# Optimization experiments

Measured on AMD Instinct MI355X. Metric: run time of the kernel, lower is better.

Reference implementation:

```python
import jax, jax.numpy as jnp
import numpy as np

D_MODEL = 1024
NUM_HEADS = 16
D_K = D_MODEL // NUM_HEADS


def setup_inputs() -> dict:
    key = jax.random.key(0)
    ks = jax.random.split(key, 11)
    B, S = 4, 2048
    scale = 1.0 / np.sqrt(D_MODEL)
    inp = {
        'query': jax.random.normal(ks[0], (B, S, D_MODEL), jnp.float32),
        'key': jax.random.normal(ks[1], (B, S, D_MODEL), jnp.float32),
        'value': jax.random.normal(ks[2], (B, S, D_MODEL), jnp.float32),
        'Wq': jax.random.normal(ks[3], (D_MODEL, D_MODEL), jnp.float32) * scale,
        'bq': jnp.zeros((D_MODEL,), jnp.float32),
        'Wk': jax.random.normal(ks[4], (D_MODEL, D_MODEL), jnp.float32) * scale,
        'bk': jnp.zeros((D_MODEL,), jnp.float32),
        'Wv': jax.random.normal(ks[5], (D_MODEL, D_MODEL), jnp.float32) * scale,
        'bv': jnp.zeros((D_MODEL,), jnp.float32),
        'Wo': jax.random.normal(ks[6], (D_MODEL, D_MODEL), jnp.float32) * scale,
        'bo': jnp.zeros((D_MODEL,), jnp.float32),
    }
    return inp


def _split_heads(x):
    # [B, S, D] -> [B, H, S, d_k]
    B, S, _ = x.shape
    return x.reshape(B, S, NUM_HEADS, D_K).transpose(0, 2, 1, 3)


def reference(query, key, value, Wq, bq, Wk, bk, Wv, bv, Wo, bo):
    # torch nn.Linear: y = x @ W.T + b
    q = _split_heads(query @ Wq.T + bq)   # [B,H,Sq,dk]
    k = _split_heads(key @ Wk.T + bk)     # [B,H,Sk,dk]
    v = _split_heads(value @ Wv.T + bv)   # [B,H,Sk,dk]
    scores = jnp.einsum('bhqd,bhkd->bhqk', q, k) / jnp.sqrt(jnp.float32(D_K))
    attn = jax.nn.softmax(scores, axis=-1)
    out = jnp.einsum('bhqk,bhkd->bhqd', attn, v)  # [B,H,Sq,dk]
    B, H, Sq, dk = out.shape
    out = out.transpose(0, 2, 1, 3).reshape(B, Sq, D_MODEL)
    return out @ Wo.T + bo
```

## Files before the change

kernel.cpp:

```cpp
#include <hip/hip_runtime.h>

typedef short bf16x8 __attribute__((ext_vector_type(8)));
typedef float f32x4 __attribute__((ext_vector_type(4)));
typedef unsigned short u16;

#define S_LEN 2048
#define DM 1024
#define NH 16
#define DK 64
#define BHD ((size_t)S_LEN * DK)

#define QSCALE 0.18033688011112042f

static __device__ __forceinline__ u16 f2bf(float f) {
  union { float f; unsigned u; } x; x.f = f;
  unsigned r = x.u + 0x7FFFu + ((x.u >> 16) & 1u);
  return (u16)(r >> 16);
}

static __device__ __forceinline__ void gload_lds16(const u16* g, u16* l) {
  __builtin_amdgcn_global_load_lds(
      (const __attribute__((address_space(1))) unsigned int*)g,
      (__attribute__((address_space(3))) unsigned int*)l, 16, 0, 0);
}

__global__ __launch_bounds__(256) void conv_all(
    const float* __restrict__ q, const float* __restrict__ k, const float* __restrict__ v,
    const float* __restrict__ Wq, const float* __restrict__ Wk,
    const float* __restrict__ Wv, const float* __restrict__ Wo,
    u16* __restrict__ xq, u16* __restrict__ xk, u16* __restrict__ xv,
    u16* __restrict__ wb) {
  const int b = blockIdx.x;
  const float* s; u16* d; float sc = 1.0f; int i;
  if (b < 8192) {
    s = q; d = xq; sc = QSCALE; i = b * 256 + threadIdx.x;
  } else if (b < 16384) {
    s = k; d = xk; i = (b - 8192) * 256 + threadIdx.x;
  } else if (b < 24576) {
    s = v; d = xv; i = (b - 16384) * 256 + threadIdx.x;
  } else {
    int b2 = b - 24576, wsel = b2 >> 10;
    s = (wsel == 0) ? Wq : (wsel == 1) ? Wk : (wsel == 2) ? Wv : Wo;
    d = wb + (size_t)wsel * 1048576;
    i = (b2 & 1023) * 256 + threadIdx.x;
  }
  float4 vv = ((const float4*)s)[i];
  ushort4 h;
  h.x = f2bf(vv.x * sc); h.y = f2bf(vv.y * sc);
  h.z = f2bf(vv.z * sc); h.w = f2bf(vv.w * sc);
  ((ushort4*)d)[i] = h;
}

#define GSTAGE(DST, SRC)                                                          \
  {                                                                               \
    _Pragma("unroll") for (int j = 0; j < 4; ++j) {                               \
      gload_lds16((SRC) + (size_t)(j * 32 + (w << 3) + (l >> 3)) * 1024 +         \
                      (size_t)(((l & 7) ^ (l >> 3)) * 8),                         \
                  (DST) + (j * 256 + w * 64) * 8);                                \
    }                                                                             \
  }

__global__ __launch_bounds__(256) void proj_gemm(
    const u16* __restrict__ xq, const u16* __restrict__ xk, const u16* __restrict__ xv,
    const u16* __restrict__ wb,
    const float* __restrict__ bq, const float* __restrict__ bk, const float* __restrict__ bv,
    u16* __restrict__ qws, u16* __restrict__ kws, u16* __restrict__ vws)
{
  __shared__ u16 Al[2][128 * 64];
  __shared__ u16 Bl[2][128 * 64];
  const int z = blockIdx.z;
  const u16* Xb = (z == 0) ? xq : (z == 1) ? xk : xv;
  const u16* Wb = wb + (size_t)z * 1048576;
  const float* bias = (z == 0) ? bq : (z == 1) ? bk : bv;
  const float bscale = (z == 0) ? QSCALE : 1.0f;

  const int t = threadIdx.x;
  const int l = t & 63, w = t >> 6;
  const int lr = l & 15, lg = l >> 4;
  const int wm = w >> 1, wn = w & 1;
  const int m0 = blockIdx.x * 128, n0 = blockIdx.y * 128;
  const int sxr = lr & 7;

  f32x4 acc[4][4] = {};

  GSTAGE(&Al[0][0], Xb + (size_t)m0 * 1024)
  GSTAGE(&Bl[0][0], Wb + (size_t)n0 * 1024)

  for (int i = 0; i < 16; ++i) {
    __syncthreads();
    if (i < 15) {
      GSTAGE(&Al[(i + 1) & 1][0], Xb + (size_t)m0 * 1024 + (i + 1) * 64)
      GSTAGE(&Bl[(i + 1) & 1][0], Wb + (size_t)n0 * 1024 + (i + 1) * 64)
    }
    const u16* Ab_ = &Al[i & 1][0];
    const u16* Bb_ = &Bl[i & 1][0];

    bf16x8 a[4][2], b[4][2];
#pragma unroll
    for (int mi = 0; mi < 4; ++mi) {
      const u16* rp = Ab_ + (wm * 64 + mi * 16 + lr) * 64;
      a[mi][0] = *(const bf16x8*)(rp + ((lg ^ sxr) * 8));
      a[mi][1] = *(const bf16x8*)(rp + (((4 + lg) ^ sxr) * 8));
    }
#pragma unroll
    for (int ni = 0; ni < 4; ++ni) {
      const u16* rp = Bb_ + (wn * 64 + ni * 16 + lr) * 64;
      b[ni][0] = *(const bf16x8*)(rp + ((lg ^ sxr) * 8));
      b[ni][1] = *(const bf16x8*)(rp + (((4 + lg) ^ sxr) * 8));
    }
    __builtin_amdgcn_s_setprio(1);
#pragma unroll
    for (int mi = 0; mi < 4; ++mi)
#pragma unroll
      for (int ni = 0; ni < 4; ++ni) {
        acc[mi][ni] = __builtin_amdgcn_mfma_f32_16x16x32_bf16(a[mi][0], b[ni][0], acc[mi][ni], 0, 0, 0);
        acc[mi][ni] = __builtin_amdgcn_mfma_f32_16x16x32_bf16(a[mi][1], b[ni][1], acc[mi][ni], 0, 0, 0);
      }
    __builtin_amdgcn_s_setprio(0);
  }

#pragma unroll
  for (int mi = 0; mi < 4; ++mi) {
#pragma unroll
    for (int ni = 0; ni < 4; ++ni) {
#pragma unroll
      for (int r = 0; r < 4; ++r) {
        int m = m0 + wm * 64 + mi * 16 + lg * 4 + r;
        int n = n0 + wn * 64 + ni * 16 + lr;
        float y = acc[mi][ni][r] + bias[n] * bscale;
        u16 h = f2bf(y);
        int b_ = m >> 11, s = m & 2047, hh = n >> 6, d = n & 63;
        size_t head = (size_t)(b_ * NH + hh);
        if (z == 0)      qws[head * BHD + (size_t)s * DK + d] = h;
        else if (z == 1) kws[head * BHD + (size_t)s * DK + d] = h;
        else             vws[head * BHD + (size_t)d * S_LEN + s] = h;
      }
    }
  }
}

__global__ __launch_bounds__(256) void oproj_gemm(
    const u16* __restrict__ Ab, const u16* __restrict__ Wob,
    const float* __restrict__ bo, float* __restrict__ out)
{
  __shared__ u16 Al[2][128 * 64];
  __shared__ u16 Bl[2][128 * 64];
  const int t = threadIdx.x;
  const int l = t & 63, w = t >> 6;
  const int lr = l & 15, lg = l >> 4;
  const int wm = w >> 1, wn = w & 1;
  const int m0 = blockIdx.x * 128, n0 = blockIdx.y * 128;
  const int sxr = lr & 7;

  f32x4 acc[4][4] = {};

  GSTAGE(&Al[0][0], Ab + (size_t)m0 * 1024)
  GSTAGE(&Bl[0][0], Wob + (size_t)n0 * 1024)

  for (int i = 0; i < 16; ++i) {
    __syncthreads();
    if (i < 15) {
      GSTAGE(&Al[(i + 1) & 1][0], Ab + (size_t)m0 * 1024 + (i + 1) * 64)
      GSTAGE(&Bl[(i + 1) & 1][0], Wob + (size_t)n0 * 1024 + (i + 1) * 64)
    }
    const u16* Ab_ = &Al[i & 1][0];
    const u16* Bb_ = &Bl[i & 1][0];

    bf16x8 a[4][2], b[4][2];
#pragma unroll
    for (int mi = 0; mi < 4; ++mi) {
      const u16* rp = Ab_ + (wm * 64 + mi * 16 + lr) * 64;
      a[mi][0] = *(const bf16x8*)(rp + ((lg ^ sxr) * 8));
      a[mi][1] = *(const bf16x8*)(rp + (((4 + lg) ^ sxr) * 8));
    }
#pragma unroll
    for (int ni = 0; ni < 4; ++ni) {
      const u16* rp = Bb_ + (wn * 64 + ni * 16 + lr) * 64;
      b[ni][0] = *(const bf16x8*)(rp + ((lg ^ sxr) * 8));
      b[ni][1] = *(const bf16x8*)(rp + (((4 + lg) ^ sxr) * 8));
    }
    __builtin_amdgcn_s_setprio(1);
#pragma unroll
    for (int mi = 0; mi < 4; ++mi)
#pragma unroll
      for (int ni = 0; ni < 4; ++ni) {
        acc[mi][ni] = __builtin_amdgcn_mfma_f32_16x16x32_bf16(a[mi][0], b[ni][0], acc[mi][ni], 0, 0, 0);
        acc[mi][ni] = __builtin_amdgcn_mfma_f32_16x16x32_bf16(a[mi][1], b[ni][1], acc[mi][ni], 0, 0, 0);
      }
    __builtin_amdgcn_s_setprio(0);
  }

#pragma unroll
  for (int mi = 0; mi < 4; ++mi) {
#pragma unroll
    for (int ni = 0; ni < 4; ++ni) {
#pragma unroll
      for (int r = 0; r < 4; ++r) {
        int m = m0 + wm * 64 + mi * 16 + lg * 4 + r;
        int n = n0 + wn * 64 + ni * 16 + lr;
        out[(size_t)m * DM + n] = acc[mi][ni][r] + bo[n];
      }
    }
  }
}

__global__ __launch_bounds__(256, 4) void attn_kernel(
    const u16* __restrict__ qh, const u16* __restrict__ kh,
    const u16* __restrict__ vt, u16* __restrict__ aout)
{
  __shared__ u16 KT[2][64 * 64];
  __shared__ u16 VT[2][64 * 64];

  const int t = threadIdx.x;
  const int l = t & 63, w = t >> 6;
  const int lr = l & 15, lg = l >> 4;

  const int bid = blockIdx.x;
  const int logical = (bid & 7) * 128 + (bid >> 3);
  const int bh = logical >> 4;
  const int qb = (logical & 15) * 128 + w * 32;

  const u16* qp = qh + (size_t)bh * BHD;
  const u16* kp = kh + (size_t)bh * BHD;
  const u16* vp = vt + (size_t)bh * BHD;
  const int sx = lr & 7;

  const int srow = t >> 3;
  const int scolS = (t & 7) ^ (srow & 7);

  bf16x8 qf[2][2];
#pragma unroll
  for (int qi = 0; qi < 2; ++qi)
#pragma unroll
    for (int c = 0; c < 2; ++c)
      qf[qi][c] = *(const bf16x8*)(qp + (size_t)(qb + qi * 16 + lr) * DK + c * 32 + lg * 8);

  bf16x8 onesf;
#pragma unroll
  for (int e = 0; e < 8; ++e) onesf[e] = (short)0x3F80;

  f32x4 acc[4][2] = {};
  f32x4 acc_l[2] = {};

#define STAGE(B, KV)                                                                  \
  {                                                                                   \
    _Pragma("unroll") for (int j = 0; j < 2; ++j) {                                   \
      gload_lds16(kp + (size_t)((KV) + j * 32 + srow) * DK + scolS * 8,               \
                  &KT[B][j * 2048 + w * 512]);                                        \
      gload_lds16(vp + (size_t)(j * 32 + srow) * S_LEN + (KV) + scolS * 8,            \
                  &VT[B][j * 2048 + w * 512]);                                        \
    }                                                                                 \
  }

  STAGE(0, 0)

  for (int i = 0; i < 32; ++i) {
    __syncthreads();
    if (i < 31) STAGE((i + 1) & 1, (i + 1) * 64)

    const u16* Kb = &KT[i & 1][0];
    const u16* Vb = &VT[i & 1][0];

    f32x4 sc[4][2] = {};
    __builtin_amdgcn_s_setprio(1);
#pragma unroll
    for (int ct = 0; ct < 4; ++ct) {
      bf16x8 k0 = *(const bf16x8*)(Kb + (ct * 16 + lr) * 64 + ((lg ^ sx) * 8));
      bf16x8 k1 = *(const bf16x8*)(Kb + (ct * 16 + lr) * 64 + (((4 + lg) ^ sx) * 8));
      sc[ct][0] = __builtin_amdgcn_mfma_f32_16x16x32_bf16(k0, qf[0][0], sc[ct][0], 0, 0, 0);
      sc[ct][0] = __builtin_amdgcn_mfma_f32_16x16x32_bf16(k1, qf[0][1], sc[ct][0], 0, 0, 0);
      sc[ct][1] = __builtin_amdgcn_mfma_f32_16x16x32_bf16(k0, qf[1][0], sc[ct][1], 0, 0, 0);
      sc[ct][1] = __builtin_amdgcn_mfma_f32_16x16x32_bf16(k1, qf[1][1], sc[ct][1], 0, 0, 0);
    }
    __builtin_amdgcn_s_setprio(0);

    unsigned cpk[2][4][2];
#pragma unroll
    for (int qi = 0; qi < 2; ++qi) {
#pragma unroll
      for (int ct = 0; ct < 4; ++ct) {
        float p0 = __builtin_amdgcn_exp2f(sc[ct][qi][0]);
        float p1 = __builtin_amdgcn_exp2f(sc[ct][qi][1]);
        float p2 = __builtin_amdgcn_exp2f(sc[ct][qi][2]);
        float p3 = __builtin_amdgcn_exp2f(sc[ct][qi][3]);
        asm("v_cvt_pk_bf16_f32 %0, %1, %2" : "=v"(cpk[qi][ct][0]) : "v"(p0), "v"(p1));
        asm("v_cvt_pk_bf16_f32 %0, %1, %2" : "=v"(cpk[qi][ct][1]) : "v"(p2), "v"(p3));
      }
    }

    bf16x8 pf[2][2];
#pragma unroll
    for (int qi = 0; qi < 2; ++qi)
#pragma unroll
      for (int kk = 0; kk < 2; ++kk) {
        unsigned a0 = cpk[qi][2 * kk][0], b0 = cpk[qi][2 * kk + 1][0];
        unsigned a1 = cpk[qi][2 * kk][1], b1 = cpk[qi][2 * kk + 1][1];
        asm("v_permlane32_swap_b32 %0, %1" : "+v"(a0), "+v"(b0));
        asm("v_permlane16_swap_b32 %0, %1" : "+v"(a0), "+v"(b0));
        asm("v_permlane32_swap_b32 %0, %1" : "+v"(a1), "+v"(b1));
        asm("v_permlane16_swap_b32 %0, %1" : "+v"(a1), "+v"(b1));
        union { unsigned u[4]; bf16x8 v; } tmp;
        tmp.u[0] = a0; tmp.u[1] = a1; tmp.u[2] = b0; tmp.u[3] = b1;
        pf[qi][kk] = tmp.v;
      }

    __builtin_amdgcn_s_setprio(1);
    acc_l[0] = __builtin_amdgcn_mfma_f32_16x16x32_bf16(pf[0][0], onesf, acc_l[0], 0, 0, 0);
    acc_l[0] = __builtin_amdgcn_mfma_f32_16x16x32_bf16(pf[0][1], onesf, acc_l[0], 0, 0, 0);
    acc_l[1] = __builtin_amdgcn_mfma_f32_16x16x32_bf16(pf[1][0], onesf, acc_l[1], 0, 0, 0);
    acc_l[1] = __builtin_amdgcn_mfma_f32_16x16x32_bf16(pf[1][1], onesf, acc_l[1], 0, 0, 0);
#pragma unroll
    for (int ni = 0; ni < 4; ++ni) {
      bf16x8 vf0 = *(const bf16x8*)(Vb + (ni * 16 + lr) * 64 + ((lg ^ sx) * 8));
      bf16x8 vf1 = *(const bf16x8*)(Vb + (ni * 16 + lr) * 64 + (((4 + lg) ^ sx) * 8));
      acc[ni][0] = __builtin_amdgcn_mfma_f32_16x16x32_bf16(pf[0][0], vf0, acc[ni][0], 0, 0, 0);
      acc[ni][0] = __builtin_amdgcn_mfma_f32_16x16x32_bf16(pf[0][1], vf1, acc[ni][0], 0, 0, 0);
      acc[ni][1] = __builtin_amdgcn_mfma_f32_16x16x32_bf16(pf[1][0], vf0, acc[ni][1], 0, 0, 0);
      acc[ni][1] = __builtin_amdgcn_mfma_f32_16x16x32_bf16(pf[1][1], vf1, acc[ni][1], 0, 0, 0);
    }
    __builtin_amdgcn_s_setprio(0);
  }
#undef STAGE

  const int b_ = bh >> 4, hh = bh & 15;
#pragma unroll
  for (int qi = 0; qi < 2; ++qi) {
#pragma unroll
    for (int r = 0; r < 4; ++r) {
      float inv = 1.0f / acc_l[qi][r];
      int s = qb + qi * 16 + lg * 4 + r;
#pragma unroll
      for (int ni = 0; ni < 4; ++ni)
        aout[((size_t)(b_ * S_LEN + s)) * DM + hh * DK + ni * 16 + lr] =
            f2bf(acc[ni][qi][r] * inv);
    }
  }
}

extern "C" void kernel_launch(void* const* d_in, const int* in_sizes, int n_in,
                              void* d_out, int out_size, void* d_ws, size_t ws_size,
                              hipStream_t stream) {
  (void)in_sizes; (void)n_in; (void)out_size; (void)ws_size;
  const float* q  = (const float*)d_in[0];
  const float* k  = (const float*)d_in[1];
  const float* v  = (const float*)d_in[2];
  const float* Wq = (const float*)d_in[3];
  const float* bq = (const float*)d_in[4];
  const float* Wk = (const float*)d_in[5];
  const float* bk = (const float*)d_in[6];
  const float* Wv = (const float*)d_in[7];
  const float* bv = (const float*)d_in[8];
  const float* Wo = (const float*)d_in[9];
  const float* bo = (const float*)d_in[10];
  float* out = (float*)d_out;

  u16* qws = (u16*)d_ws;
  u16* kws = qws + (size_t)8388608;
  u16* vws = kws + (size_t)8388608;
  u16* xb  = vws + (size_t)8388608;
  u16* wb  = xb  + (size_t)8388608;
  u16* aws = xb;
  u16* kxb = (u16*)d_out;
  u16* vxb = kxb + (size_t)8388608;

  conv_all<<<dim3(28672), dim3(256), 0, stream>>>(q, k, v, Wq, Wk, Wv, Wo, xb, kxb, vxb, wb);

  proj_gemm<<<dim3(64, 8, 3), dim3(256), 0, stream>>>(xb, kxb, vxb, wb, bq, bk, bv,
                                                      qws, kws, vws);

  attn_kernel<<<dim3(1024), dim3(256), 0, stream>>>(qws, kws, vws, aws);

  oproj_gemm<<<dim3(64, 8), dim3(256), 0, stream>>>(aws, wb + 3145728, bo, out);
}
```

Before: 198.4 us.

## Fuse fp32-to-bf16 activation conversion into the projection GEMM's A-tile staging

```diff
diff --git a/kernel.cpp b/kernel.cpp
--- a/kernel.cpp
+++ b/kernel.cpp
@@ -24,26 +24,16 @@
       (__attribute__((address_space(3))) unsigned int*)l, 16, 0, 0);
 }
 
-__global__ __launch_bounds__(256) void conv_all(
-    const float* __restrict__ q, const float* __restrict__ k, const float* __restrict__ v,
+__global__ __launch_bounds__(256) void conv_w(
     const float* __restrict__ Wq, const float* __restrict__ Wk,
     const float* __restrict__ Wv, const float* __restrict__ Wo,
-    u16* __restrict__ xq, u16* __restrict__ xk, u16* __restrict__ xv,
     u16* __restrict__ wb) {
   const int b = blockIdx.x;
-  const float* s; u16* d; float sc = 1.0f; int i;
-  if (b < 8192) {
-    s = q; d = xq; sc = QSCALE; i = b * 256 + threadIdx.x;
-  } else if (b < 16384) {
-    s = k; d = xk; i = (b - 8192) * 256 + threadIdx.x;
-  } else if (b < 24576) {
-    s = v; d = xv; i = (b - 16384) * 256 + threadIdx.x;
-  } else {
-    int b2 = b - 24576, wsel = b2 >> 10;
-    s = (wsel == 0) ? Wq : (wsel == 1) ? Wk : (wsel == 2) ? Wv : Wo;
-    d = wb + (size_t)wsel * 1048576;
-    i = (b2 & 1023) * 256 + threadIdx.x;
-  }
+  const int wsel = b >> 10;
+  const float* s = (wsel == 0) ? Wq : (wsel == 1) ? Wk : (wsel == 2) ? Wv : Wo;
+  const float sc = (wsel == 0) ? QSCALE : 1.0f;
+  u16* d = wb + (size_t)wsel * 1048576;
+  int i = (b & 1023) * 256 + threadIdx.x;
   float4 vv = ((const float4*)s)[i];
   ushort4 h;
   h.x = f2bf(vv.x * sc); h.y = f2bf(vv.y * sc);
@@ -60,16 +50,39 @@
     }                                                                             \
   }
 
+#define ASTAGE_LOAD(R, SRCF, K0)                                                  \
+  {                                                                               \
+    _Pragma("unroll") for (int j = 0; j < 4; ++j) {                               \
+      const int r_ = j * 32 + (t >> 3);                                           \
+      const int g_ = (t & 7) ^ (r_ & 7);                                          \
+      const float* p_ = (SRCF) + (size_t)(m0 + r_) * 1024 + (K0) + g_ * 8;        \
+      R[j][0] = *(const float4*)(p_);                                             \
+      R[j][1] = *(const float4*)(p_ + 4);                                         \
+    }                                                                             \
+  }
+#define ASTAGE_WRITE(DST, R)                                                      \
+  {                                                                               \
+    _Pragma("unroll") for (int j = 0; j < 4; ++j) {                               \
+      unsigned u0, u1, u2, u3;                                                    \
+      asm("v_cvt_pk_bf16_f32 %0, %1, %2" : "=v"(u0) : "v"(R[j][0].x), "v"(R[j][0].y)); \
+      asm("v_cvt_pk_bf16_f32 %0, %1, %2" : "=v"(u1) : "v"(R[j][0].z), "v"(R[j][0].w)); \
+      asm("v_cvt_pk_bf16_f32 %0, %1, %2" : "=v"(u2) : "v"(R[j][1].x), "v"(R[j][1].y)); \
+      asm("v_cvt_pk_bf16_f32 %0, %1, %2" : "=v"(u3) : "v"(R[j][1].z), "v"(R[j][1].w)); \
+      uint4 pk_; pk_.x = u0; pk_.y = u1; pk_.z = u2; pk_.w = u3;                  \
+      *(uint4*)((DST) + (size_t)(t + j * 256) * 8) = pk_;                         \
+    }                                                                             \
+  }
+
 __global__ __launch_bounds__(256) void proj_gemm(
-    const u16* __restrict__ xq, const u16* __restrict__ xk, const u16* __restrict__ xv,
-    const u16* __restrict__ wb,
+    const float* __restrict__ qf32, const float* __restrict__ kf32,
+    const float* __restrict__ vf32, const u16* __restrict__ wb,
     const float* __restrict__ bq, const float* __restrict__ bk, const float* __restrict__ bv,
     u16* __restrict__ qws, u16* __restrict__ kws, u16* __restrict__ vws)
 {
   __shared__ u16 Al[2][128 * 64];
   __shared__ u16 Bl[2][128 * 64];
   const int z = blockIdx.z;
-  const u16* Xb = (z == 0) ? xq : (z == 1) ? xk : xv;
+  const float* Xf = (z == 0) ? qf32 : (z == 1) ? kf32 : vf32;
   const u16* Wb = wb + (size_t)z * 1048576;
   const float* bias = (z == 0) ? bq : (z == 1) ? bk : bv;
   const float bscale = (z == 0) ? QSCALE : 1.0f;
@@ -82,14 +95,16 @@
   const int sxr = lr & 7;
 
   f32x4 acc[4][4] = {};
-
-  GSTAGE(&Al[0][0], Xb + (size_t)m0 * 1024)
+  float4 areg[4][2];
+
+  ASTAGE_LOAD(areg, Xf, 0)
   GSTAGE(&Bl[0][0], Wb + (size_t)n0 * 1024)
+  ASTAGE_WRITE(&Al[0][0], areg)
 
   for (int i = 0; i < 16; ++i) {
     __syncthreads();
     if (i < 15) {
-      GSTAGE(&Al[(i + 1) & 1][0], Xb + (size_t)m0 * 1024 + (i + 1) * 64)
+      ASTAGE_LOAD(areg, Xf, (i + 1) * 64)
       GSTAGE(&Bl[(i + 1) & 1][0], Wb + (size_t)n0 * 1024 + (i + 1) * 64)
     }
     const u16* Ab_ = &Al[i & 1][0];
@@ -117,6 +132,8 @@
         acc[mi][ni] = __builtin_amdgcn_mfma_f32_16x16x32_bf16(a[mi][1], b[ni][1], acc[mi][ni], 0, 0, 0);
       }
     __builtin_amdgcn_s_setprio(0);
+
+    if (i < 15) ASTAGE_WRITE(&Al[(i + 1) & 1][0], areg)
   }
 
 #pragma unroll
@@ -357,15 +374,12 @@
   u16* qws = (u16*)d_ws;
   u16* kws = qws + (size_t)8388608;
   u16* vws = kws + (size_t)8388608;
-  u16* xb  = vws + (size_t)8388608;
-  u16* wb  = xb  + (size_t)8388608;
-  u16* aws = xb;
-  u16* kxb = (u16*)d_out;
-  u16* vxb = kxb + (size_t)8388608;
-
-  conv_all<<<dim3(28672), dim3(256), 0, stream>>>(q, k, v, Wq, Wk, Wv, Wo, xb, kxb, vxb, wb);
-
-  proj_gemm<<<dim3(64, 8, 3), dim3(256), 0, stream>>>(xb, kxb, vxb, wb, bq, bk, bv,
+  u16* aws = vws + (size_t)8388608;
+  u16* wb  = aws + (size_t)8388608;
+
+  conv_w<<<dim3(4096), dim3(256), 0, stream>>>(Wq, Wk, Wv, Wo, wb);
+
+  proj_gemm<<<dim3(64, 8, 3), dim3(256), 0, stream>>>(q, k, v, wb, bq, bk, bv,
                                                       qws, kws, vws);
 
   attn_kernel<<<dim3(1024), dim3(256), 0, stream>>>(qws, kws, vws, aws);
```

New measurement: 197.5 us. Within noise of the previous version (-0.4%).
